# Optimization experiments

Measured on AMD Instinct MI355X. Metric: run time of the kernel, lower is better.

Reference implementation:

```python
import jax, jax.numpy as jnp
import numpy as np

KS = 3          # kernel_size
NUM_FA = 16     # number of functional atoms per pixel
TOTAL_BASES = 6 # num_bases * (ks // 2)
BN_EPS = 1e-5


def _conv3x3(x, w, b):
    # NCHW conv, padding=1, stride=1
    y = jax.lax.conv_general_dilated(
        x, w, window_strides=(1, 1), padding=[(1, 1), (1, 1)],
        dimension_numbers=("NCHW", "OIHW", "NCHW"))
    return y + b[None, :, None, None]


def _bn(x, gamma, beta, mean, var):
    scale = gamma / jnp.sqrt(var + BN_EPS)
    return (x - mean[None, :, None, None]) * scale[None, :, None, None] + beta[None, :, None, None]


def setup_inputs() -> dict:
    key = jax.random.key(0)
    ks = jax.random.split(key, 16)
    N, C, H, W = 16, 64, 64, 64
    INTER, BC_DIM, O = 64, TOTAL_BASES * NUM_FA, 128
    f32 = jnp.float32
    return {
        "x": jax.random.normal(ks[0], (N, C, H, W), f32),
        "conv1_w": jax.random.normal(ks[1], (INTER, C, 3, 3), f32) * 0.05,
        "conv1_b": jax.random.normal(ks[2], (INTER,), f32) * 0.05,
        "bn1_gamma": jax.random.uniform(ks[3], (INTER,), f32, 0.5, 1.5),
        "bn1_beta": jax.random.normal(ks[4], (INTER,), f32) * 0.05,
        "bn1_mean": jax.random.normal(ks[5], (INTER,), f32) * 0.05,
        "bn1_var": jax.random.uniform(ks[6], (INTER,), f32, 0.5, 1.5),
        "conv2_w": jax.random.normal(ks[7], (BC_DIM, INTER, 3, 3), f32) * 0.05,
        "conv2_b": jax.random.normal(ks[8], (BC_DIM,), f32) * 0.05,
        "bn2_gamma": jax.random.uniform(ks[9], (BC_DIM,), f32, 0.5, 1.5),
        "bn2_beta": jax.random.normal(ks[10], (BC_DIM,), f32) * 0.05,
        "bn2_mean": jax.random.normal(ks[11], (BC_DIM,), f32) * 0.05,
        "bn2_var": jax.random.uniform(ks[12], (BC_DIM,), f32, 0.5, 1.5),
        "bases": jax.random.normal(ks[13], (TOTAL_BASES, KS * KS), f32),
        "coef": jax.random.normal(ks[14], (O, C * NUM_FA), f32) * 0.02,
    }


def reference(x, conv1_w, conv1_b, bn1_gamma, bn1_beta, bn1_mean, bn1_var,
              conv2_w, conv2_b, bn2_gamma, bn2_beta, bn2_mean, bn2_var,
              bases, coef):
    N, C, H, W = x.shape
    # bases_net: conv3x3 -> BN -> tanh -> conv3x3 -> BN -> tanh
    h = jnp.tanh(_bn(_conv3x3(x, conv1_w, conv1_b), bn1_gamma, bn1_beta, bn1_mean, bn1_var))
    bc = jnp.tanh(_bn(_conv3x3(h, conv2_w, conv2_b), bn2_gamma, bn2_beta, bn2_mean, bn2_var))
    # torch: .transpose(1,-1).view(N,H,W,num_fa,total_bases)  (swaps H/W; H==W)
    bases_coef = jnp.transpose(bc, (0, 3, 2, 1)).reshape(N, H, W, NUM_FA, TOTAL_BASES)
    # atoms: (bases_coef[...,None] * bases).sum(-2).transpose(-1,-2) -> (N,H,W,ks2,num_fa)
    atoms = jnp.einsum("nhwft,tk->nhwkf", bases_coef, bases)
    # unfold(x, ks, padding=1) -> patches (N,H,W,C,ks2), channel-major like torch unfold
    xp = jnp.pad(x, ((0, 0), (0, 0), (1, 1), (1, 1)))
    patches = jnp.stack([xp[:, :, i:i + H, j:j + W] for i in range(KS) for j in range(KS)], axis=2)  # (N,C,9,H,W)
    patches = jnp.transpose(patches, (0, 3, 4, 1, 2))  # (N,H,W,C,9)
    # (x.unsqueeze(-1) * atoms.unsqueeze(-3)).sum(-2) -> (N,H,W,C,num_fa) -> flatten C-major
    bases_out = jnp.einsum("nhwck,nhwkf->nhwcf", patches, atoms).reshape(N, H, W, C * NUM_FA)
    # torch: .transpose(1,-1) -> (N, C*num_fa, W, H), then 1x1 conv with coef
    out = jnp.einsum("nhwd,od->nowh", bases_out, coef)  # (N, O, W, H)
    return out
```

## Files before the change

kernel.cpp:

```cpp
#include <hip/hip_runtime.h>
#include <math.h>
#include <string.h>

#define NBATCH 16

typedef __attribute__((ext_vector_type(8))) short short8;
typedef __attribute__((ext_vector_type(4))) float floatx4;
#define MFMA16(a, b, c) __builtin_amdgcn_mfma_f32_16x16x32_bf16(a, b, c, 0, 0, 0)

__device__ __forceinline__ unsigned short f2bf(float f) {
  unsigned int u = __float_as_uint(f);
  unsigned int rounding = ((u >> 16) & 1u) + 0x7fffu;
  return (unsigned short)((u + rounding) >> 16);
}
__device__ __forceinline__ unsigned int packbf2(float a, float b) {
  return (unsigned int)f2bf(a) | ((unsigned int)f2bf(b) << 16);
}
__device__ __forceinline__ float bflo(unsigned int u) {
  return __uint_as_float(u << 16);
}
__device__ __forceinline__ float bfhi(unsigned int u) {
  return __uint_as_float(u & 0xffff0000u);
}
__device__ __forceinline__ float fast_tanh(float x) {
  float e = __expf(2.f * x);
  return 1.f - 2.f / (e + 1.f);
}

__global__ void prep_weights(const float* __restrict__ w1,
                             const float* __restrict__ w2,
                             const float* __restrict__ coef,
                             unsigned short* __restrict__ w1swz,
                             unsigned short* __restrict__ w2swz,
                             unsigned short* __restrict__ coefswz) {
  int i = blockIdx.x * 256 + threadIdx.x;
  if (i < 131072) {
    int j = i & 7, f = i >> 3;
    int lane = f & 63;
    int u = (f >> 6) & 7;
    int kc = (f >> 9) & 1;
    int rd = f >> 10;
    int lm = lane & 15, lq = lane >> 4;
    int oc = u * 16 + lm;
    int k = rd * 64 + kc * 32 + lq * 8 + j;
    coefswz[i] = f2bf(coef[oc * 1024 + k]);
  }
  if (i < 36864) {
    int j = i & 7, f = i >> 3;
    int lane = f & 63;
    int u = (f >> 6) & 1;
    int wn = (f >> 7) & 1;
    int kc = (f >> 8) & 1;
    int off = f >> 9;
    int lm = lane & 15, lq = lane >> 4;
    int oc = wn * 32 + u * 16 + lm;
    int ic = kc * 32 + lq * 8 + j;
    w1swz[i] = f2bf(w1[(oc * 64 + ic) * 9 + off]);
  }
  if (i < 55296) {
    int j = i & 7, f = i >> 3;
    int lane = f & 63;
    int rem = f >> 6;
    int u = rem % 3;
    int rem2 = rem / 3;
    int wn = rem2 & 1;
    int kc = (rem2 >> 1) & 1;
    int off = rem2 >> 2;
    int lm = lane & 15, lq = lane >> 4;
    int oc = wn * 48 + u * 16 + lm;
    int ic = kc * 32 + lq * 8 + j;
    w2swz[i] = f2bf(w2[(oc * 64 + ic) * 9 + off]);
  }
}

__global__ __launch_bounds__(256) void xb_prep(const float* __restrict__ x,
                                               unsigned short* __restrict__ xb) {
  __shared__ float tile[64][65];
  const int t = threadIdx.x;
  const int y = blockIdx.x, n = blockIdx.y;
  const float* xn = x + (size_t)n * 64 * 4096 + y * 64;
#pragma unroll
  for (int it = 0; it < 16; ++it) {
    int idx = it * 256 + t;
    int c = idx >> 6, xx = idx & 63;
    tile[c][xx] = xn[c * 4096 + xx];
  }
  __syncthreads();
  const int xx = t >> 2, cq = t & 3;
  unsigned short* dst = xb + ((size_t)n * 4096 + y * 64 + xx) * 64;
#pragma unroll
  for (int jj = 0; jj < 2; ++jj) {
    int ch0 = cq * 16 + jj * 8;
    unsigned int p[4];
#pragma unroll
    for (int e = 0; e < 4; ++e)
      p[e] = packbf2(tile[ch0 + e * 2][xx], tile[ch0 + e * 2 + 1][xx]);
    *(uint4*)&dst[ch0] = make_uint4(p[0], p[1], p[2], p[3]);
  }
}

__global__ __launch_bounds__(256) void fused_conv(
    const unsigned short* __restrict__ xb, const unsigned short* __restrict__ w1swz,
    const unsigned short* __restrict__ w2swz, const float* __restrict__ b1,
    const float* __restrict__ g1, const float* __restrict__ be1,
    const float* __restrict__ m1, const float* __restrict__ v1,
    const float* __restrict__ b2, const float* __restrict__ g2,
    const float* __restrict__ be2, const float* __restrict__ m2,
    const float* __restrict__ v2, unsigned short* __restrict__ bcg) {
  __shared__ unsigned short xls[240 * 72];
  __shared__ unsigned short hls[192 * 72];

  const int t = threadIdx.x;
  const int tile = blockIdx.x, n = blockIdx.y;
  const int x0 = (tile & 3) * 16, y0 = (tile >> 2) * 8;

  const unsigned short* xbn = xb + (size_t)n * 4096 * 64;
#pragma unroll
  for (int it = 0; it < 8; ++it) {
    int idx = it * 256 + t;
    if (idx < 1920) {
      int pos = idx >> 3, u4 = idx & 7;
      int xr = pos / 20, xc = pos - xr * 20;
      int gy = y0 - 2 + xr, gx = x0 - 2 + xc;
      uint4 v = {0u, 0u, 0u, 0u};
      if ((unsigned)gy < 64u && (unsigned)gx < 64u)
        v = *(const uint4*)&xbn[((size_t)gy * 64 + gx) * 64 + u4 * 8];
      *(uint4*)&xls[pos * 72 + u4 * 8] = v;
    }
  }
  __syncthreads();

  const int lane = t & 63, w = t >> 6;
  const int wm = w & 1, wn = w >> 1;
  const int lm = lane & 15, lq = lane >> 4;

  int abase[6];
#pragma unroll
  for (int i = 0; i < 6; ++i) {
    int m = wm + 2 * i;
    int px = m * 16 + lm;
    if (px > 179) px = 179;
    int r = px / 18, c = px - r * 18;
    abase[i] = (r * 20 + c) * 72 + lq * 8;
  }
  floatx4 acc[6][2];
#pragma unroll
  for (int i = 0; i < 6; ++i)
#pragma unroll
    for (int u = 0; u < 2; ++u) acc[i][u] = floatx4{0.f, 0.f, 0.f, 0.f};

#pragma unroll
  for (int step = 0; step < 18; ++step) {
    const int off = step >> 1, kc = step & 1;
    const int di = off / 3, dj = off % 3;
    short8 b[2];
#pragma unroll
    for (int u = 0; u < 2; ++u)
      b[u] = *(const short8*)&w1swz[(off * 512 + kc * 256 + wn * 128 + u * 64 +
                                     lane) * 8];
#pragma unroll
    for (int i = 0; i < 6; ++i) {
      short8 a = *(const short8*)&xls[abase[i] + (di * 20 + dj) * 72 + kc * 32];
      acc[i][0] = MFMA16(a, b[0], acc[i][0]);
      acc[i][1] = MFMA16(a, b[1], acc[i][1]);
    }
  }
  {
    float sc[2], sh[2];
#pragma unroll
    for (int u = 0; u < 2; ++u) {
      int oc = wn * 32 + u * 16 + lm;
      sc[u] = g1[oc] * rsqrtf(v1[oc] + 1e-5f);
      sh[u] = (b1[oc] - m1[oc]) * sc[u] + be1[oc];
    }
#pragma unroll
    for (int i = 0; i < 6; ++i) {
      int px0 = (wm + 2 * i) * 16 + lq * 4;
#pragma unroll
      for (int u = 0; u < 2; ++u) {
        int oc = wn * 32 + u * 16 + lm;
#pragma unroll
        for (int r = 0; r < 4; ++r) {
          int px = px0 + r;
          int rh = px / 18, ch = px - rh * 18;
          int gy = y0 - 1 + rh, gx = x0 - 1 + ch;
          bool valid = ((unsigned)gy < 64u) && ((unsigned)gx < 64u);
          float val = valid ? fast_tanh(acc[i][u][r] * sc[u] + sh[u]) : 0.f;
          hls[px * 72 + oc] = f2bf(val);
        }
      }
    }
  }
  __syncthreads();

  int hbase[4];
#pragma unroll
  for (int i = 0; i < 4; ++i) {
    int opx = (wm + 2 * i) * 16 + lm;
    int br = opx >> 4, bcol = opx & 15;
    hbase[i] = (br * 18 + bcol) * 72 + lq * 8;
  }
  floatx4 acc2[4][3];
#pragma unroll
  for (int i = 0; i < 4; ++i)
#pragma unroll
    for (int u = 0; u < 3; ++u) acc2[i][u] = floatx4{0.f, 0.f, 0.f, 0.f};

#pragma unroll
  for (int step = 0; step < 18; ++step) {
    const int off = step >> 1, kc = step & 1;
    const int di = off / 3, dj = off % 3;
    short8 b[3];
#pragma unroll
    for (int u = 0; u < 3; ++u)
      b[u] = *(const short8*)&w2swz[(off * 768 + kc * 384 + wn * 192 + u * 64 +
                                     lane) * 8];
#pragma unroll
    for (int i = 0; i < 4; ++i) {
      short8 a = *(const short8*)&hls[hbase[i] + (di * 18 + dj) * 72 + kc * 32];
      acc2[i][0] = MFMA16(a, b[0], acc2[i][0]);
      acc2[i][1] = MFMA16(a, b[1], acc2[i][1]);
      acc2[i][2] = MFMA16(a, b[2], acc2[i][2]);
    }
  }
  {
    float sc[3], sh[3];
#pragma unroll
    for (int u = 0; u < 3; ++u) {
      int oc = wn * 48 + u * 16 + lm;
      sc[u] = g2[oc] * rsqrtf(v2[oc] + 1e-5f);
      sh[u] = (b2[oc] - m2[oc]) * sc[u] + be2[oc];
    }
    unsigned short* bcn = bcg + (size_t)n * 4096 * 96;
#pragma unroll
    for (int i = 0; i < 4; ++i) {
      int opx0 = (wm + 2 * i) * 16 + lq * 4;
#pragma unroll
      for (int u = 0; u < 3; ++u) {
        int oc = wn * 48 + u * 16 + lm;
#pragma unroll
        for (int r = 0; r < 4; ++r) {
          int opx = opx0 + r;
          int y = y0 + (opx >> 4), xx = x0 + (opx & 15);
          bcn[((size_t)y * 64 + xx) * 96 + oc] =
              f2bf(fast_tanh(acc2[i][u][r] * sc[u] + sh[u]));
        }
      }
    }
  }
}

__global__ __launch_bounds__(256) void adconv_final(
    const unsigned short* __restrict__ xb, const unsigned short* __restrict__ bc,
    const float* __restrict__ bases, const unsigned short* __restrict__ coefswz,
    float* __restrict__ out) {
  __shared__ unsigned short xs[100 * 72];

  const int t = threadIdx.x;
  const int tile = blockIdx.x, n = blockIdx.y;
  const int q0 = (tile & 7) * 8, p0 = (tile >> 3) * 8;

  float bs[54];
#pragma unroll
  for (int i = 0; i < 54; ++i) bs[i] = bases[i];

  const unsigned short* xbn = xb + (size_t)n * 4096 * 64;
#pragma unroll
  for (int it = 0; it < 4; ++it) {
    int idx = it * 256 + t;
    if (idx < 800) {
      int pos = idx >> 3, u4 = idx & 7;
      int r = pos / 10, col = pos - r * 10;
      int gp = p0 - 1 + r, gq = q0 - 1 + col;
      uint4 v = {0u, 0u, 0u, 0u};
      if ((unsigned)gp < 64u && (unsigned)gq < 64u)
        v = *(const uint4*)&xbn[((size_t)gp * 64 + gq) * 64 + u4 * 8];
      *(uint4*)&xs[pos * 72 + u4 * 8] = v;
    }
  }

  const int lane = t & 63, w = t >> 6;
  const int lm = lane & 15, lq = lane >> 4;
  const int px = w * 16 + lm;
  const int qx = px >> 3, py = px & 7;
  const int fh = lq & 1;
  const unsigned sh = (lq >> 1) * 16;

  float at[9][8];
  {
    const unsigned short* bp =
        bc + ((size_t)n * 4096 + (q0 + qx) * 64 + (p0 + py)) * 96 + fh * 48;
    float bcv[48];
#pragma unroll
    for (int m = 0; m < 6; ++m) {
      uint4 v = *(const uint4*)(bp + m * 8);
      unsigned int uu[4] = {v.x, v.y, v.z, v.w};
#pragma unroll
      for (int e = 0; e < 4; ++e) {
        bcv[m * 8 + e * 2] = bflo(uu[e]);
        bcv[m * 8 + e * 2 + 1] = bfhi(uu[e]);
      }
    }
#pragma unroll
    for (int j = 0; j < 8; ++j)
#pragma unroll
      for (int k = 0; k < 9; ++k) {
        float a = 0.f;
#pragma unroll
        for (int tt = 0; tt < 6; ++tt)
          a = fmaf(bcv[j * 6 + tt], bs[tt * 9 + k], a);
        at[k][j] = a;
      }
  }

  int pa[9];
#pragma unroll
  for (int i = 0; i < 3; ++i)
#pragma unroll
    for (int j = 0; j < 3; ++j)
      pa[i * 3 + j] = ((py + i) * 10 + qx + j) * 72;

  const unsigned short* cbase = coefswz + (size_t)lane * 8;

  __syncthreads();

  floatx4 acc[8];
#pragma unroll
  for (int u = 0; u < 8; ++u) acc[u] = floatx4{0.f, 0.f, 0.f, 0.f};

#pragma unroll
  for (int rd = 0; rd < 16; ++rd) {
    uint2 q[9];
#pragma unroll
    for (int p = 0; p < 9; ++p) q[p] = *(const uint2*)&xs[pa[p] + rd * 4];
    float a0[8], a1[8];
#pragma unroll
    for (int j = 0; j < 8; ++j) { a0[j] = 0.f; a1[j] = 0.f; }
#pragma unroll
    for (int p = 0; p < 9; ++p) {
      float p0v = __uint_as_float((q[p].x >> sh) << 16);
      float p1v = __uint_as_float((q[p].y >> sh) << 16);
#pragma unroll
      for (int j = 0; j < 8; ++j) {
        a0[j] = fmaf(p0v, at[p][j], a0[j]);
        a1[j] = fmaf(p1v, at[p][j], a1[j]);
      }
    }
    short8 A0, A1;
    {
      unsigned int w0[4], w1[4];
#pragma unroll
      for (int e = 0; e < 4; ++e) {
        w0[e] = packbf2(a0[e * 2], a0[e * 2 + 1]);
        w1[e] = packbf2(a1[e * 2], a1[e * 2 + 1]);
      }
      uint4 t0 = make_uint4(w0[0], w0[1], w0[2], w0[3]);
      uint4 t1 = make_uint4(w1[0], w1[1], w1[2], w1[3]);
      A0 = *(short8*)&t0;
      A1 = *(short8*)&t1;
    }
#pragma unroll
    for (int u = 0; u < 8; ++u) {
      short8 b0 = *(const short8*)(cbase + (size_t)(rd * 1024 + u * 64) * 8);
      short8 b1 =
          *(const short8*)(cbase + (size_t)(rd * 1024 + 512 + u * 64) * 8);
      acc[u] = MFMA16(A0, b0, acc[u]);
      acc[u] = MFMA16(A1, b1, acc[u]);
    }
  }

  float* outn = out + (size_t)n * 128 * 4096;
  const int px0 = w * 16 + lq * 4;
  const int qxs = px0 >> 3, py0 = px0 & 7;
#pragma unroll
  for (int u = 0; u < 8; ++u) {
    int oc = u * 16 + lm;
    *(float4*)&outn[((size_t)oc * 64 + q0 + qxs) * 64 + p0 + py0] =
        make_float4(acc[u][0], acc[u][1], acc[u][2], acc[u][3]);
  }
}

extern "C" void kernel_launch(void* const* d_in, const int* in_sizes, int n_in,
                              void* d_out, int out_size, void* d_ws,
                              size_t ws_size, hipStream_t stream) {
  const float* x = (const float*)d_in[0];
  const float* conv1_w = (const float*)d_in[1];
  const float* conv1_b = (const float*)d_in[2];
  const float* bn1_g = (const float*)d_in[3];
  const float* bn1_b = (const float*)d_in[4];
  const float* bn1_m = (const float*)d_in[5];
  const float* bn1_v = (const float*)d_in[6];
  const float* conv2_w = (const float*)d_in[7];
  const float* conv2_b = (const float*)d_in[8];
  const float* bn2_g = (const float*)d_in[9];
  const float* bn2_b = (const float*)d_in[10];
  const float* bn2_m = (const float*)d_in[11];
  const float* bn2_v = (const float*)d_in[12];
  const float* bases = (const float*)d_in[13];
  const float* coef = (const float*)d_in[14];
  float* out = (float*)d_out;

  char* ws = (char*)d_ws;
  unsigned short* xbuf = (unsigned short*)(ws);
  unsigned short* bcb = (unsigned short*)(ws + 8388608);
  unsigned short* w1swz = (unsigned short*)(ws + 20971520);
  unsigned short* w2swz = (unsigned short*)(ws + 21045248);
  unsigned short* coefswz = (unsigned short*)(ws + 21155840);

  prep_weights<<<512, 256, 0, stream>>>(conv1_w, conv2_w, coef, w1swz, w2swz,
                                        coefswz);
  xb_prep<<<dim3(64, NBATCH), 256, 0, stream>>>(x, xbuf);
  fused_conv<<<dim3(32, NBATCH), 256, 0, stream>>>(
      xbuf, w1swz, w2swz, conv1_b, bn1_g, bn1_b, bn1_m, bn1_v, conv2_b, bn2_g,
      bn2_b, bn2_m, bn2_v, bcb);
  adconv_final<<<dim3(64, NBATCH), 256, 0, stream>>>(xbuf, bcb, bases, coefswz,
                                                     out);
}
```

Measured before the change: 188.4 us.

## Shrink fused_conv tiles and restructure adconv_final with shared-memory A tiles

fused_conv moves from 16x8 to 8x8 output tiles, which doubles the grid and cuts shared memory use, at the price of more halo recomputation for conv1. adconv_final now handles 128-pixel tiles. Each thread builds the atom-weighted patch products for half a pixel and writes them into double-buffered shared memory. The four waves then split the MFMA work as 2 pixel halves by 2 output-channel halves, so each coef fragment is loaded once per block and reused across four pixel subtiles. The coef swizzle is reordered to match, and the A-tile build for the next step overlaps the current MFMAs, with one barrier per step.

```diff
diff --git a/kernel.cpp b/kernel.cpp
--- a/kernel.cpp
+++ b/kernel.cpp
@@ -37,11 +37,12 @@
   if (i < 131072) {
     int j = i & 7, f = i >> 3;
     int lane = f & 63;
-    int u = (f >> 6) & 7;
+    int u = (f >> 6) & 3;
+    int wj = (f >> 8) & 1;
     int kc = (f >> 9) & 1;
     int rd = f >> 10;
     int lm = lane & 15, lq = lane >> 4;
-    int oc = u * 16 + lm;
+    int oc = wj * 64 + u * 16 + lm;
     int k = rd * 64 + kc * 32 + lq * 8 + j;
     coefswz[i] = f2bf(coef[oc * 1024 + k]);
   }
@@ -107,20 +108,20 @@
     const float* __restrict__ b2, const float* __restrict__ g2,
     const float* __restrict__ be2, const float* __restrict__ m2,
     const float* __restrict__ v2, unsigned short* __restrict__ bcg) {
-  __shared__ unsigned short xls[240 * 72];
-  __shared__ unsigned short hls[192 * 72];
+  __shared__ unsigned short xls[144 * 72];
+  __shared__ unsigned short hls[128 * 72];
 
   const int t = threadIdx.x;
   const int tile = blockIdx.x, n = blockIdx.y;
-  const int x0 = (tile & 3) * 16, y0 = (tile >> 2) * 8;
+  const int x0 = (tile & 7) * 8, y0 = (tile >> 3) * 8;
 
   const unsigned short* xbn = xb + (size_t)n * 4096 * 64;
 #pragma unroll
-  for (int it = 0; it < 8; ++it) {
+  for (int it = 0; it < 5; ++it) {
     int idx = it * 256 + t;
-    if (idx < 1920) {
+    if (idx < 1152) {
       int pos = idx >> 3, u4 = idx & 7;
-      int xr = pos / 20, xc = pos - xr * 20;
+      int xr = pos / 12, xc = pos - xr * 12;
       int gy = y0 - 2 + xr, gx = x0 - 2 + xc;
       uint4 v = {0u, 0u, 0u, 0u};
       if ((unsigned)gy < 64u && (unsigned)gx < 64u)
@@ -134,18 +135,17 @@
   const int wm = w & 1, wn = w >> 1;
   const int lm = lane & 15, lq = lane >> 4;
 
-  int abase[6];
-#pragma unroll
-  for (int i = 0; i < 6; ++i) {
-    int m = wm + 2 * i;
-    int px = m * 16 + lm;
-    if (px > 179) px = 179;
-    int r = px / 18, c = px - r * 18;
-    abase[i] = (r * 20 + c) * 72 + lq * 8;
-  }
-  floatx4 acc[6][2];
-#pragma unroll
-  for (int i = 0; i < 6; ++i)
+  int abase[4];
+#pragma unroll
+  for (int i = 0; i < 4; ++i) {
+    int px = (wm + 2 * i) * 16 + lm;
+    if (px > 99) px = 99;
+    int hr = px / 10, hc = px - hr * 10;
+    abase[i] = (hr * 12 + hc) * 72 + lq * 8;
+  }
+  floatx4 acc[4][2];
+#pragma unroll
+  for (int i = 0; i < 4; ++i)
 #pragma unroll
     for (int u = 0; u < 2; ++u) acc[i][u] = floatx4{0.f, 0.f, 0.f, 0.f};
 
@@ -159,8 +159,8 @@
       b[u] = *(const short8*)&w1swz[(off * 512 + kc * 256 + wn * 128 + u * 64 +
                                      lane) * 8];
 #pragma unroll
-    for (int i = 0; i < 6; ++i) {
-      short8 a = *(const short8*)&xls[abase[i] + (di * 20 + dj) * 72 + kc * 32];
+    for (int i = 0; i < 4; ++i) {
+      short8 a = *(const short8*)&xls[abase[i] + (di * 12 + dj) * 72 + kc * 32];
       acc[i][0] = MFMA16(a, b[0], acc[i][0]);
       acc[i][1] = MFMA16(a, b[1], acc[i][1]);
     }
@@ -174,7 +174,7 @@
       sh[u] = (b1[oc] - m1[oc]) * sc[u] + be1[oc];
     }
 #pragma unroll
-    for (int i = 0; i < 6; ++i) {
+    for (int i = 0; i < 4; ++i) {
       int px0 = (wm + 2 * i) * 16 + lq * 4;
 #pragma unroll
       for (int u = 0; u < 2; ++u) {
@@ -182,29 +182,31 @@
 #pragma unroll
         for (int r = 0; r < 4; ++r) {
           int px = px0 + r;
-          int rh = px / 18, ch = px - rh * 18;
-          int gy = y0 - 1 + rh, gx = x0 - 1 + ch;
-          bool valid = ((unsigned)gy < 64u) && ((unsigned)gx < 64u);
-          float val = valid ? fast_tanh(acc[i][u][r] * sc[u] + sh[u]) : 0.f;
-          hls[px * 72 + oc] = f2bf(val);
+          if (px < 100) {
+            int hr = px / 10, hc = px - hr * 10;
+            int gy = y0 - 1 + hr, gx = x0 - 1 + hc;
+            bool valid = ((unsigned)gy < 64u) && ((unsigned)gx < 64u);
+            float val = valid ? fast_tanh(acc[i][u][r] * sc[u] + sh[u]) : 0.f;
+            hls[px * 72 + oc] = f2bf(val);
+          }
         }
       }
     }
   }
   __syncthreads();
 
-  int hbase[4];
-#pragma unroll
-  for (int i = 0; i < 4; ++i) {
-    int opx = (wm + 2 * i) * 16 + lm;
-    int br = opx >> 4, bcol = opx & 15;
-    hbase[i] = (br * 18 + bcol) * 72 + lq * 8;
-  }
-  floatx4 acc2[4][3];
-#pragma unroll
-  for (int i = 0; i < 4; ++i)
-#pragma unroll
-    for (int u = 0; u < 3; ++u) acc2[i][u] = floatx4{0.f, 0.f, 0.f, 0.f};
+  int hbase[2];
+#pragma unroll
+  for (int s = 0; s < 2; ++s) {
+    int opx = (wm + 2 * s) * 16 + lm;
+    int yl = opx >> 3, xl = opx & 7;
+    hbase[s] = (yl * 10 + xl) * 72 + lq * 8;
+  }
+  floatx4 acc2[2][3];
+#pragma unroll
+  for (int s = 0; s < 2; ++s)
+#pragma unroll
+    for (int u = 0; u < 3; ++u) acc2[s][u] = floatx4{0.f, 0.f, 0.f, 0.f};
 
 #pragma unroll
   for (int step = 0; step < 18; ++step) {
@@ -216,11 +218,11 @@
       b[u] = *(const short8*)&w2swz[(off * 768 + kc * 384 + wn * 192 + u * 64 +
                                      lane) * 8];
 #pragma unroll
-    for (int i = 0; i < 4; ++i) {
-      short8 a = *(const short8*)&hls[hbase[i] + (di * 18 + dj) * 72 + kc * 32];
-      acc2[i][0] = MFMA16(a, b[0], acc2[i][0]);
-      acc2[i][1] = MFMA16(a, b[1], acc2[i][1]);
-      acc2[i][2] = MFMA16(a, b[2], acc2[i][2]);
+    for (int s = 0; s < 2; ++s) {
+      short8 a = *(const short8*)&hls[hbase[s] + (di * 10 + dj) * 72 + kc * 32];
+      acc2[s][0] = MFMA16(a, b[0], acc2[s][0]);
+      acc2[s][1] = MFMA16(a, b[1], acc2[s][1]);
+      acc2[s][2] = MFMA16(a, b[2], acc2[s][2]);
     }
   }
   {
@@ -233,32 +235,33 @@
     }
     unsigned short* bcn = bcg + (size_t)n * 4096 * 96;
 #pragma unroll
-    for (int i = 0; i < 4; ++i) {
-      int opx0 = (wm + 2 * i) * 16 + lq * 4;
+    for (int s = 0; s < 2; ++s) {
+      int opx0 = (wm + 2 * s) * 16 + lq * 4;
 #pragma unroll
       for (int u = 0; u < 3; ++u) {
         int oc = wn * 48 + u * 16 + lm;
 #pragma unroll
         for (int r = 0; r < 4; ++r) {
           int opx = opx0 + r;
-          int y = y0 + (opx >> 4), xx = x0 + (opx & 15);
+          int y = y0 + (opx >> 3), xx = x0 + (opx & 7);
           bcn[((size_t)y * 64 + xx) * 96 + oc] =
-              f2bf(fast_tanh(acc2[i][u][r] * sc[u] + sh[u]));
+              f2bf(fast_tanh(acc2[s][u][r] * sc[u] + sh[u]));
         }
       }
     }
   }
 }
 
-__global__ __launch_bounds__(256) void adconv_final(
+__global__ __launch_bounds__(256, 2) void adconv_final(
     const unsigned short* __restrict__ xb, const unsigned short* __restrict__ bc,
     const float* __restrict__ bases, const unsigned short* __restrict__ coefswz,
     float* __restrict__ out) {
-  __shared__ unsigned short xs[100 * 72];
+  __shared__ unsigned short xs[180 * 72];
+  __shared__ uint4 As2[2 * 128 * 9];
 
   const int t = threadIdx.x;
   const int tile = blockIdx.x, n = blockIdx.y;
-  const int q0 = (tile & 7) * 8, p0 = (tile >> 3) * 8;
+  const int q0 = (tile & 3) * 16, p0 = (tile >> 2) * 8;
 
   float bs[54];
 #pragma unroll
@@ -266,12 +269,12 @@
 
   const unsigned short* xbn = xb + (size_t)n * 4096 * 64;
 #pragma unroll
-  for (int it = 0; it < 4; ++it) {
+  for (int it = 0; it < 6; ++it) {
     int idx = it * 256 + t;
-    if (idx < 800) {
+    if (idx < 1440) {
       int pos = idx >> 3, u4 = idx & 7;
-      int r = pos / 10, col = pos - r * 10;
-      int gp = p0 - 1 + r, gq = q0 - 1 + col;
+      int row = pos / 18, col = pos - row * 18;
+      int gp = p0 - 1 + row, gq = q0 - 1 + col;
       uint4 v = {0u, 0u, 0u, 0u};
       if ((unsigned)gp < 64u && (unsigned)gq < 64u)
         v = *(const uint4*)&xbn[((size_t)gp * 64 + gq) * 64 + u4 * 8];
@@ -281,15 +284,15 @@
 
   const int lane = t & 63, w = t >> 6;
   const int lm = lane & 15, lq = lane >> 4;
-  const int px = w * 16 + lm;
-  const int qx = px >> 3, py = px & 7;
-  const int fh = lq & 1;
-  const unsigned sh = (lq >> 1) * 16;
+  const int wi = w & 1, wj = w >> 1;
+
+  const int px_a = t >> 1, fh = t & 1;
+  const int qx_a = px_a >> 3, py_a = px_a & 7;
 
   float at[9][8];
   {
     const unsigned short* bp =
-        bc + ((size_t)n * 4096 + (q0 + qx) * 64 + (p0 + py)) * 96 + fh * 48;
+        bc + ((size_t)n * 4096 + (q0 + qx_a) * 64 + (p0 + py_a)) * 96 + fh * 48;
     float bcv[48];
 #pragma unroll
     for (int m = 0; m < 6; ++m) {
@@ -318,65 +321,92 @@
   for (int i = 0; i < 3; ++i)
 #pragma unroll
     for (int j = 0; j < 3; ++j)
-      pa[i * 3 + j] = ((py + i) * 10 + qx + j) * 72;
-
-  const unsigned short* cbase = coefswz + (size_t)lane * 8;
+      pa[i * 3 + j] = ((py_a + i) * 18 + qx_a + j) * 72;
+
+  floatx4 acc[4][4];
+#pragma unroll
+  for (int s = 0; s < 4; ++s)
+#pragma unroll
+    for (int u = 0; u < 4; ++u) acc[s][u] = floatx4{0.f, 0.f, 0.f, 0.f};
+
+  auto build = [&](int rd, int buf) {
+    const int coff = rd * 4;
+    uint2 q[9];
+#pragma unroll
+    for (int p = 0; p < 9; ++p) q[p] = *(const uint2*)&xs[pa[p] + coff];
+    float a[4][8];
+#pragma unroll
+    for (int cc = 0; cc < 4; ++cc)
+#pragma unroll
+      for (int jj = 0; jj < 8; ++jj) a[cc][jj] = 0.f;
+#pragma unroll
+    for (int p = 0; p < 9; ++p) {
+      float c0 = bflo(q[p].x), c1 = bfhi(q[p].x);
+      float c2 = bflo(q[p].y), c3 = bfhi(q[p].y);
+#pragma unroll
+      for (int jj = 0; jj < 8; ++jj) {
+        float av = at[p][jj];
+        a[0][jj] = fmaf(c0, av, a[0][jj]);
+        a[1][jj] = fmaf(c1, av, a[1][jj]);
+        a[2][jj] = fmaf(c2, av, a[2][jj]);
+        a[3][jj] = fmaf(c3, av, a[3][jj]);
+      }
+    }
+    uint4* dst = &As2[buf * 1152 + px_a * 9];
+#pragma unroll
+    for (int cc = 0; cc < 4; ++cc) {
+      int unit = (cc >> 1) * 4 + (cc & 1) * 2 + fh;
+      dst[unit] = make_uint4(packbf2(a[cc][0], a[cc][1]),
+                             packbf2(a[cc][2], a[cc][3]),
+                             packbf2(a[cc][4], a[cc][5]),
+                             packbf2(a[cc][6], a[cc][7]));
+    }
+  };
 
   __syncthreads();
-
-  floatx4 acc[8];
-#pragma unroll
-  for (int u = 0; u < 8; ++u) acc[u] = floatx4{0.f, 0.f, 0.f, 0.f};
-
-#pragma unroll
+  build(0, 0);
+  __syncthreads();
+
   for (int rd = 0; rd < 16; ++rd) {
-    uint2 q[9];
-#pragma unroll
-    for (int p = 0; p < 9; ++p) q[p] = *(const uint2*)&xs[pa[p] + rd * 4];
-    float a0[8], a1[8];
-#pragma unroll
-    for (int j = 0; j < 8; ++j) { a0[j] = 0.f; a1[j] = 0.f; }
-#pragma unroll
-    for (int p = 0; p < 9; ++p) {
-      float p0v = __uint_as_float((q[p].x >> sh) << 16);
-      float p1v = __uint_as_float((q[p].y >> sh) << 16);
-#pragma unroll
-      for (int j = 0; j < 8; ++j) {
-        a0[j] = fmaf(p0v, at[p][j], a0[j]);
-        a1[j] = fmaf(p1v, at[p][j], a1[j]);
-      }
-    }
-    short8 A0, A1;
-    {
-      unsigned int w0[4], w1[4];
-#pragma unroll
-      for (int e = 0; e < 4; ++e) {
-        w0[e] = packbf2(a0[e * 2], a0[e * 2 + 1]);
-        w1[e] = packbf2(a1[e * 2], a1[e * 2 + 1]);
-      }
-      uint4 t0 = make_uint4(w0[0], w0[1], w0[2], w0[3]);
-      uint4 t1 = make_uint4(w1[0], w1[1], w1[2], w1[3]);
-      A0 = *(short8*)&t0;
-      A1 = *(short8*)&t1;
-    }
-#pragma unroll
-    for (int u = 0; u < 8; ++u) {
-      short8 b0 = *(const short8*)(cbase + (size_t)(rd * 1024 + u * 64) * 8);
-      short8 b1 =
-          *(const short8*)(cbase + (size_t)(rd * 1024 + 512 + u * 64) * 8);
-      acc[u] = MFMA16(A0, b0, acc[u]);
-      acc[u] = MFMA16(A1, b1, acc[u]);
-    }
+    const int buf = rd & 1;
+    short8 Af[4][2];
+#pragma unroll
+    for (int s = 0; s < 4; ++s) {
+      int px = wi * 64 + s * 16 + lm;
+#pragma unroll
+      for (int kc = 0; kc < 2; ++kc)
+        Af[s][kc] = *(const short8*)&As2[buf * 1152 + px * 9 + kc * 4 + lq];
+    }
+    short8 Bf[2][4];
+#pragma unroll
+    for (int kc = 0; kc < 2; ++kc)
+#pragma unroll
+      for (int u = 0; u < 4; ++u) {
+        int frag = ((rd * 2 + kc) * 2 + wj) * 4 + u;
+        Bf[kc][u] = *(const short8*)(coefswz + ((size_t)frag * 64 + lane) * 8);
+      }
+    if (rd < 15) build(rd + 1, buf ^ 1);
+#pragma unroll
+    for (int kc = 0; kc < 2; ++kc)
+#pragma unroll
+      for (int u = 0; u < 4; ++u)
+#pragma unroll
+        for (int s = 0; s < 4; ++s)
+          acc[s][u] = MFMA16(Af[s][kc], Bf[kc][u], acc[s][u]);
+    __syncthreads();
   }
 
   float* outn = out + (size_t)n * 128 * 4096;
-  const int px0 = w * 16 + lq * 4;
-  const int qxs = px0 >> 3, py0 = px0 & 7;
-#pragma unroll
-  for (int u = 0; u < 8; ++u) {
-    int oc = u * 16 + lm;
-    *(float4*)&outn[((size_t)oc * 64 + q0 + qxs) * 64 + p0 + py0] =
-        make_float4(acc[u][0], acc[u][1], acc[u][2], acc[u][3]);
+#pragma unroll
+  for (int u = 0; u < 4; ++u) {
+    int oc = wj * 64 + u * 16 + lm;
+#pragma unroll
+    for (int s = 0; s < 4; ++s) {
+      int px0 = wi * 64 + s * 16 + lq * 4;
+      int qx = px0 >> 3, py0 = px0 & 7;
+      *(float4*)&outn[((size_t)oc * 64 + q0 + qx) * 64 + p0 + py0] =
+          make_float4(acc[s][u][0], acc[s][u][1], acc[s][u][2], acc[s][u][3]);
+    }
   }
 }
 
@@ -410,9 +440,9 @@
   prep_weights<<<512, 256, 0, stream>>>(conv1_w, conv2_w, coef, w1swz, w2swz,
                                         coefswz);
   xb_prep<<<dim3(64, NBATCH), 256, 0, stream>>>(x, xbuf);
-  fused_conv<<<dim3(32, NBATCH), 256, 0, stream>>>(
+  fused_conv<<<dim3(64, NBATCH), 256, 0, stream>>>(
       xbuf, w1swz, w2swz, conv1_b, bn1_g, bn1_b, bn1_m, bn1_v, conv2_b, bn2_g,
       bn2_b, bn2_m, bn2_v, bcb);
-  adconv_final<<<dim3(64, NBATCH), 256, 0, stream>>>(xbuf, bcb, bases, coefswz,
+  adconv_final<<<dim3(32, NBATCH), 256, 0, stream>>>(xbuf, bcb, bases, coefswz,
                                                      out);
 }
```

Result: faster. 167.2 us (-11.3%).
